# Kernel tuning notes

Measured on AMD Instinct MI355X. Metric: run time of the kernel, lower is better.

Reference implementation:

```python
import jax, jax.numpy as jnp
import numpy as np

# Constants from the torch module
S_DECAY = 0.95    # sentence_decay
P_DECAY = 0.99    # paragraph_decay
D_DECAY = 0.999   # document_decay
ALPHA = 0.1       # delta_update alpha for sentence/paragraph
DOC_ALPHA = 0.05  # delta_update alpha for document
BETA = 1.0
PARA_GROUP = 5    # sentences per paragraph
EPS = 1e-12       # F.normalize eps


def _normalize(x):
    # matches torch.nn.functional.normalize(x, dim=-1)
    return x / jnp.maximum(jnp.linalg.norm(x, axis=-1, keepdims=True), EPS)


def _delta_step(M, kn, v, alpha, beta):
    # M: [H, dk, dv]; kn: [dk] (already L2-normalized); v: [dv]
    # M_new = M @ (I - alpha * kn kn^T) + beta * kn v^T   (erase matrix is symmetric,
    # so the einsum 'hkv,hkj->hjv' form equals this rank-1 update -- no dk x dk matrix needed)
    kTM = jnp.einsum('k,hkv->hv', kn, M)                       # [H, dv]
    return M - alpha * kn[None, :, None] * kTM[:, None, :] \
             + beta * (kn[:, None] * v[None, :])[None, :, :]


def _scan_updates(M0, K, V, decay, alpha, beta):
    # Streaming delta-rule: per step, decay then erase/write.
    def step(M, kv):
        k, v = kv
        M = M * decay
        M = _delta_step(M, _normalize(k), v, alpha, beta)
        return M, None
    M, _ = jax.lax.scan(step, M0, (K, V))
    return M


def setup_inputs() -> dict:
    key = jax.random.key(0)
    ks = jax.random.split(key, 7)
    T, d_emb, d_k, d_v, H = 1000, 768, 256, 256, 8
    emb = jax.random.normal(ks[0], (T, d_emb), dtype=jnp.float32)
    q = jax.random.normal(ks[1], (d_k,), dtype=jnp.float32)
    W_k = jax.random.normal(ks[2], (d_emb, d_k), dtype=jnp.float32) * 0.02
    b_k = jax.random.normal(ks[3], (d_k,), dtype=jnp.float32) * 0.02
    W_v = jax.random.normal(ks[4], (d_emb, d_v), dtype=jnp.float32) * 0.02
    b_v = jax.random.normal(ks[5], (d_v,), dtype=jnp.float32) * 0.02
    M_sent0 = jnp.zeros((H, d_k, d_v), dtype=jnp.float32)
    M_para0 = jnp.zeros((H, d_k, d_v), dtype=jnp.float32)
    M_doc0 = jnp.zeros((H, d_k, d_v), dtype=jnp.float32)
    return {"emb": emb, "q": q, "W_k": W_k, "b_k": b_k, "W_v": W_v, "b_v": b_v,
            "M_sent0": M_sent0, "M_para0": M_para0, "M_doc0": M_doc0}


def reference(emb, q, W_k, b_k, W_v, b_v, M_sent0, M_para0, M_doc0):
    T, d_emb = emb.shape
    # Level 1: sentence memory -- one delta update per sentence embedding
    K = emb @ W_k + b_k            # [T, dk]
    V = emb @ W_v + b_v            # [T, dv]
    M_sent = _scan_updates(M_sent0, K, V, S_DECAY, ALPHA, BETA)
    # Level 2: paragraph memory -- mean of each group of 5 sentence embeddings
    para_emb = emb.reshape(T // PARA_GROUP, PARA_GROUP, d_emb).mean(axis=1)
    PK = para_emb @ W_k + b_k
    PV = para_emb @ W_v + b_v
    M_para = _scan_updates(M_para0, PK, PV, P_DECAY, ALPHA, BETA)
    # Level 3: document memory -- single update from paragraph-memory statistics
    doc_k = M_para.mean(axis=0).mean(axis=-1)   # [dk]
    doc_v = M_para.mean(axis=0).mean(axis=0)    # [dv]
    M_doc = M_doc0 * D_DECAY
    M_doc = _delta_step(M_doc, _normalize(doc_k), doc_v, DOC_ALPHA, BETA)
    # recall(q, level='all')
    qn = _normalize(q)
    def recall(M):
        return jnp.einsum('hkv,k->hv', M, qn).mean(axis=0)   # [dv]
    return 0.2 * recall(M_sent) + 0.3 * recall(M_para) + 0.5 * recall(M_doc)
```

## Files before the change

kernel.cpp:

```cpp
#include <hip/hip_runtime.h>
#include <hip/hip_bf16.h>

#define ALPHA   0.1f
#define S_DECAY 0.95f
#define P_DECAY 0.99f
#define D_EMB   768
#define DK      256

template<int ctrl, int row_mask>
__device__ __forceinline__ float dpp_add(float x) {
    int y = __builtin_amdgcn_update_dpp(0, __float_as_int(x), ctrl, row_mask, 0xF, true);
    return x + __int_as_float(y);
}

template<int N>
__device__ __forceinline__ void wave_allred_arr(float (&x)[N]) {
#pragma unroll
    for (int n = 0; n < N; ++n) x[n] = dpp_add<0xB1,  0xF>(x[n]);
#pragma unroll
    for (int n = 0; n < N; ++n) x[n] = dpp_add<0x4E,  0xF>(x[n]);
#pragma unroll
    for (int n = 0; n < N; ++n) x[n] = dpp_add<0x141, 0xF>(x[n]);
#pragma unroll
    for (int n = 0; n < N; ++n) x[n] = dpp_add<0x140, 0xF>(x[n]);
#pragma unroll
    for (int n = 0; n < N; ++n) x[n] = dpp_add<0x142, 0xA>(x[n]);
#pragma unroll
    for (int n = 0; n < N; ++n) x[n] = dpp_add<0x143, 0xC>(x[n]);
#pragma unroll
    for (int n = 0; n < N; ++n)
        x[n] = __int_as_float(__builtin_amdgcn_readlane(__float_as_int(x[n]), 63));
}

__device__ __forceinline__ float dot4v(const float4& a, const float4& b) {
    float t0 = a.x * b.x; t0 = fmaf(a.y, b.y, t0);
    float t1 = a.z * b.z; t1 = fmaf(a.w, b.w, t1);
    return t0 + t1;
}

__device__ __forceinline__ float rl(float x, int lane) {
    return __int_as_float(__builtin_amdgcn_readlane(__float_as_int(x), lane));
}

__global__ __launch_bounds__(256) void prep_kernel(
    const float* __restrict__ emb,
    const float* __restrict__ Wk, const float* __restrict__ bk,
    const float* __restrict__ Wv, const float* __restrict__ bv,
    float* __restrict__ K, float* __restrict__ V, float* __restrict__ USrev,
    float* __restrict__ out, int T)
{
    const int tid = threadIdx.x;
    const int bid = blockIdx.x;
    const int NBLK = (T / 4) * 2;
    if (bid >= NBLK) {
        const int PADS = ((T + 63) / 64) * 64;
        for (int i = tid; i < (PADS - T) * DK; i += 256) USrev[(size_t)T * DK + i] = 0.f;
        out[tid] = 0.f;
        return;
    }
    const int mat = bid & 1;
    const int r0  = (bid >> 1) * 4;

    __shared__ float se[4][D_EMB];
    __shared__ float s_red[4][4];

    const float4* emb4 = reinterpret_cast<const float4*>(emb);
#pragma unroll
    for (int r = 0; r < 4; ++r) {
        if (tid < D_EMB / 4)
            reinterpret_cast<float4*>(se[r])[tid] = emb4[(size_t)(r0 + r) * (D_EMB / 4) + tid];
    }
    __syncthreads();

    const float* Wp = mat ? Wv : Wk;
    const float* bp = mat ? bv : bk;
    const int j = tid;

    float a0 = 0.f, a1 = 0.f, a2 = 0.f, a3 = 0.f;
    float c0 = Wp[j],        c1 = Wp[j + DK],     c2 = Wp[j + 2*DK], c3 = Wp[j + 3*DK];
    float p0 = Wp[j + 4*DK], p1 = Wp[j + 5*DK],   p2 = Wp[j + 6*DK], p3 = Wp[j + 7*DK];

    for (int d = 0; d < D_EMB; d += 4) {
        int dn = d + 8; if (dn >= D_EMB) dn = 0;
        const float* wn = Wp + (size_t)dn * DK + j;
        float n0 = wn[0], n1 = wn[DK], n2 = wn[2*DK], n3 = wn[3*DK];

        float4 e0 = *reinterpret_cast<const float4*>(&se[0][d]);
        float4 e1 = *reinterpret_cast<const float4*>(&se[1][d]);
        float4 e2 = *reinterpret_cast<const float4*>(&se[2][d]);
        float4 e3 = *reinterpret_cast<const float4*>(&se[3][d]);

        a0 = fmaf(e0.x, c0, a0); a0 = fmaf(e0.y, c1, a0);
        a0 = fmaf(e0.z, c2, a0); a0 = fmaf(e0.w, c3, a0);
        a1 = fmaf(e1.x, c0, a1); a1 = fmaf(e1.y, c1, a1);
        a1 = fmaf(e1.z, c2, a1); a1 = fmaf(e1.w, c3, a1);
        a2 = fmaf(e2.x, c0, a2); a2 = fmaf(e2.y, c1, a2);
        a2 = fmaf(e2.z, c2, a2); a2 = fmaf(e2.w, c3, a2);
        a3 = fmaf(e3.x, c0, a3); a3 = fmaf(e3.y, c1, a3);
        a3 = fmaf(e3.z, c2, a3); a3 = fmaf(e3.w, c3, a3);

        c0 = p0; c1 = p1; c2 = p2; c3 = p3;
        p0 = n0; p1 = n1; p2 = n2; p3 = n3;
    }

    float bj = bp[j];
    float o0 = a0 + bj, o1 = a1 + bj, o2 = a2 + bj, o3 = a3 + bj;
    float* dst = mat ? V : K;
    dst[(size_t)(r0 + 0) * DK + j] = o0;
    dst[(size_t)(r0 + 1) * DK + j] = o1;
    dst[(size_t)(r0 + 2) * DK + j] = o2;
    dst[(size_t)(r0 + 3) * DK + j] = o3;

    if (mat == 0) {
        const int wave = tid >> 6, l = tid & 63;
        float red[4] = { o0*o0, o1*o1, o2*o2, o3*o3 };
        wave_allred_arr(red);
        if (l == 0) {
            s_red[wave][0] = red[0]; s_red[wave][1] = red[1];
            s_red[wave][2] = red[2]; s_red[wave][3] = red[3];
        }
        __syncthreads();
        float t0 = s_red[0][0] + s_red[1][0] + s_red[2][0] + s_red[3][0];
        float t1 = s_red[0][1] + s_red[1][1] + s_red[2][1] + s_red[3][1];
        float t2 = s_red[0][2] + s_red[1][2] + s_red[2][2] + s_red[3][2];
        float t3 = s_red[0][3] + s_red[1][3] + s_red[2][3] + s_red[3][3];
        USrev[(size_t)(T - 1 - (r0 + 0)) * DK + j] = o0 * (1.0f / fmaxf(sqrtf(t0), 1e-12f));
        USrev[(size_t)(T - 1 - (r0 + 1)) * DK + j] = o1 * (1.0f / fmaxf(sqrtf(t1), 1e-12f));
        USrev[(size_t)(T - 1 - (r0 + 2)) * DK + j] = o2 * (1.0f / fmaxf(sqrtf(t2), 1e-12f));
        USrev[(size_t)(T - 1 - (r0 + 3)) * DK + j] = o3 * (1.0f / fmaxf(sqrtf(t3), 1e-12f));
    }
}

__global__ __launch_bounds__(256) void graminv_kernel(
    const float* __restrict__ K, const float* __restrict__ V,
    const float* __restrict__ USrev,
    float* __restrict__ UPrev, float* __restrict__ UPfwd,
    float* __restrict__ PV, float* __restrict__ SVv,
    float* __restrict__ AinvT, float* __restrict__ biasF,
    int P, int NCS, int NCP)
{
    __shared__ float sU[64 * 257];
    __shared__ float sA[64 * 65];
    __shared__ float sX[64 * 65];
    __shared__ float s_sv[64];
    __shared__ float s_pd[64];
    const int tid = threadIdx.x, wv = tid >> 6, l = tid & 63;
    const int bid = blockIdx.x;
    int type, m;
    if (bid < NCS)            { type = 0; m = bid; }
    else if (bid < NCS + NCP) { type = 1; m = bid - NCS; }
    else                      { type = 2; m = bid - NCS - NCP; }

    if (tid < 64) s_pd[tid] = powf(P_DECAY, (float)tid);

    if (type == 0) {
        const float4* U4 = reinterpret_cast<const float4*>(USrev) + (size_t)m * 4096;
        for (int idx = tid; idx < 4096; idx += 256) {
            float4 t = U4[idx];
            int row = idx >> 6, c4 = (idx & 63) << 2;
            float* b = &sU[row * 257 + c4];
            b[0] = t.x; b[1] = t.y; b[2] = t.z; b[3] = t.w;
        }
    } else if (type == 1) {
        const float4* K4 = reinterpret_cast<const float4*>(K);
        for (int ii = 0; ii < 16; ++ii) {
            int i = wv * 16 + ii;
            int p = P - 1 - (64 * m + i);
            float4 u = make_float4(0.f, 0.f, 0.f, 0.f);
            if (p >= 0) {
                float4 pk = make_float4(0.f, 0.f, 0.f, 0.f);
#pragma unroll
                for (int s = 0; s < 5; ++s) {
                    float4 k4 = K4[(size_t)(5 * p + s) * 64 + l];
                    pk.x += k4.x; pk.y += k4.y; pk.z += k4.z; pk.w += k4.w;
                }
                pk.x *= 0.2f; pk.y *= 0.2f; pk.z *= 0.2f; pk.w *= 0.2f;
                float red[1] = { dot4v(pk, pk) };
                wave_allred_arr(red);
                float inv = 1.0f / fmaxf(sqrtf(red[0]), 1e-12f);
                u = make_float4(pk.x * inv, pk.y * inv, pk.z * inv, pk.w * inv);
            }
            float* b = &sU[i * 257 + 4 * l];
            b[0] = u.x; b[1] = u.y; b[2] = u.z; b[3] = u.w;
            reinterpret_cast<float4*>(UPrev)[(size_t)(64 * m + i) * 64 + l] = u;
        }
    } else {
        const float4* K4 = reinterpret_cast<const float4*>(K);
        const float4* V4 = reinterpret_cast<const float4*>(V);
        for (int ii = 0; ii < 16; ++ii) {
            int i = wv * 16 + ii;
            int p = 64 * m + i;
            float4 u = make_float4(0.f, 0.f, 0.f, 0.f);
            float sv = 0.f;
            if (p < P) {
                float4 pk = make_float4(0.f, 0.f, 0.f, 0.f);
                float4 pv = make_float4(0.f, 0.f, 0.f, 0.f);
#pragma unroll
                for (int s = 0; s < 5; ++s) {
                    float4 k4 = K4[(size_t)(5 * p + s) * 64 + l];
                    float4 v4 = V4[(size_t)(5 * p + s) * 64 + l];
                    pk.x += k4.x; pk.y += k4.y; pk.z += k4.z; pk.w += k4.w;
                    pv.x += v4.x; pv.y += v4.y; pv.z += v4.z; pv.w += v4.w;
                }
                pk.x *= 0.2f; pk.y *= 0.2f; pk.z *= 0.2f; pk.w *= 0.2f;
                pv.x *= 0.2f; pv.y *= 0.2f; pv.z *= 0.2f; pv.w *= 0.2f;
                reinterpret_cast<float4*>(PV)[(size_t)p * 64 + l] = pv;
                float red[2] = { dot4v(pk, pk), pv.x + pv.y + pv.z + pv.w };
                wave_allred_arr(red);
                float inv = 1.0f / fmaxf(sqrtf(red[0]), 1e-12f);
                u = make_float4(pk.x * inv, pk.y * inv, pk.z * inv, pk.w * inv);
                sv = red[1];
            }
            float* b = &sU[i * 257 + 4 * l];
            b[0] = u.x; b[1] = u.y; b[2] = u.z; b[3] = u.w;
            reinterpret_cast<float4*>(UPfwd)[(size_t)(64 * m + i) * 64 + l] = u;
            if (l == 0) { s_sv[i] = sv; SVv[64 * m + i] = sv; }
        }
    }
    __syncthreads();

    const int tr = tid & 15, tcg = tid >> 4;
    const int i0 = tr * 4, j0 = tcg * 4;
    float g00=0,g01=0,g02=0,g03=0, g10=0,g11=0,g12=0,g13=0;
    float g20=0,g21=0,g22=0,g23=0, g30=0,g31=0,g32=0,g33=0;
    for (int k = 0; k < 256; ++k) {
        float aa0 = sU[(i0    ) * 257 + k];
        float aa1 = sU[(i0 + 1) * 257 + k];
        float aa2 = sU[(i0 + 2) * 257 + k];
        float aa3 = sU[(i0 + 3) * 257 + k];
        float bb0 = sU[(j0    ) * 257 + k];
        float bb1 = sU[(j0 + 1) * 257 + k];
        float bb2 = sU[(j0 + 2) * 257 + k];
        float bb3 = sU[(j0 + 3) * 257 + k];
        g00 = fmaf(aa0, bb0, g00); g01 = fmaf(aa0, bb1, g01);
        g02 = fmaf(aa0, bb2, g02); g03 = fmaf(aa0, bb3, g03);
        g10 = fmaf(aa1, bb0, g10); g11 = fmaf(aa1, bb1, g11);
        g12 = fmaf(aa1, bb2, g12); g13 = fmaf(aa1, bb3, g13);
        g20 = fmaf(aa2, bb0, g20); g21 = fmaf(aa2, bb1, g21);
        g22 = fmaf(aa2, bb2, g22); g23 = fmaf(aa2, bb3, g23);
        g30 = fmaf(aa3, bb0, g30); g31 = fmaf(aa3, bb1, g31);
        g32 = fmaf(aa3, bb2, g32); g33 = fmaf(aa3, bb3, g33);
    }
    float gt[4][4] = { {g00,g01,g02,g03}, {g10,g11,g12,g13},
                       {g20,g21,g22,g23}, {g30,g31,g32,g33} };
#pragma unroll
    for (int r = 0; r < 4; ++r)
#pragma unroll
        for (int c = 0; c < 4; ++c) {
            int gi = i0 + r, gj = j0 + c;
            float val = 0.f;
            if (gj < gi) {
                val = ALPHA * gt[r][c];
                if (type == 2) val *= s_pd[gi - gj];
            }
            sA[gi * 65 + gj] = val;
        }
    __syncthreads();

    if (type == 2 && wv == 0) {
        float dotb = 0.f;
#pragma unroll
        for (int jj = 0; jj < 64; ++jj)
            dotb = fmaf(sA[l * 65 + jj], s_sv[jj], dotb);
        biasF[m * 64 + l] = dotb * (1.0f / ALPHA);
    }

    const int base = wv * 16;
    float x[16];
#pragma unroll
    for (int r = 0; r < 16; ++r) x[r] = (base + r == l) ? 1.f : 0.f;
    for (int s = 0; s < 4; ++s) {
        if (wv == s) {
#pragma unroll
            for (int i = 1; i < 16; ++i)
#pragma unroll
                for (int jj = 0; jj < 16; ++jj)
                    if (jj < i)
                        x[i] = fmaf(-sA[(base + i) * 65 + (base + jj)], x[jj], x[i]);
#pragma unroll
            for (int r = 0; r < 16; ++r) sX[(base + r) * 65 + l] = x[r];
        }
        __syncthreads();
        if (wv > s) {
#pragma unroll
            for (int i = 0; i < 16; ++i) {
                float xi = sX[(s * 16 + i) * 65 + l];
#pragma unroll
                for (int r = 0; r < 16; ++r)
                    x[r] = fmaf(-sA[(base + r) * 65 + (s * 16 + i)], xi, x[r]);
            }
        }
    }
    __syncthreads();
    float* dstA = AinvT + (size_t)bid * 4096;
    for (int idx = tid; idx < 4096; idx += 256) {
        int jcol = idx >> 6, irow = idx & 63;
        dstA[idx] = sX[irow * 65 + jcol];
    }
}

__global__ __launch_bounds__(256) void solve_kernel(
    const float* __restrict__ USrev, const float* __restrict__ UPrev,
    const float* __restrict__ UPfwd, const float* __restrict__ SVv,
    const float* __restrict__ AinvT, const float* __restrict__ biasF,
    const float* __restrict__ q,
    float* __restrict__ CS, float* __restrict__ CPB1, float* __restrict__ CPB2,
    float* __restrict__ gscal, int NCS, int NCP)
{
    __shared__ float s_b1[64], s_b2[64];
    __shared__ float4 s_part[4][64], s_part2[4][64];
    __shared__ float sAinv[4096];
    __shared__ float s_powd[65];
    const int tid = threadIdx.x, wave = tid >> 6, l = tid & 63;
    const int wbase = wave * 16;
    if (tid <= 64) s_powd[tid] = powf(P_DECAY, (float)tid);

    float4 q4 = reinterpret_cast<const float4*>(q)[l];
    float qs[1] = { dot4v(q4, q4) };
    wave_allred_arr(qs);
    float qinv = 1.0f / fmaxf(sqrtf(qs[0]), 1e-12f);
    float4 qn = make_float4(q4.x * qinv, q4.y * qinv, q4.z * qinv, q4.w * qinv);
    __syncthreads();

    const float4* G4 = reinterpret_cast<const float4*>(AinvT);
    float4* sAinv4 = reinterpret_cast<float4*>(sAinv);

    if (blockIdx.x == 0) {
        float4 w1 = qn;
        const float4* U4 = reinterpret_cast<const float4*>(USrev);
        float4 cur[16];
#pragma unroll
        for (int r = 0; r < 16; ++r) cur[r] = U4[(size_t)(wbase + r) * 64 + l];
        for (int m = 0; m < NCS; ++m) {
            float4 g0 = G4[(size_t)m * 1024 + 0*256 + tid];
            float4 g1 = G4[(size_t)m * 1024 + 1*256 + tid];
            float4 g2 = G4[(size_t)m * 1024 + 2*256 + tid];
            float4 g3 = G4[(size_t)m * 1024 + 3*256 + tid];
            float4 nxt[16];
            if (m + 1 < NCS) {
                const float4* Un = U4 + (size_t)(m + 1) * 64 * 64;
#pragma unroll
                for (int r = 0; r < 16; ++r) nxt[r] = Un[(size_t)(wbase + r) * 64 + l];
            }
#pragma unroll
            for (int g = 0; g < 4; ++g) {
                float d[4];
#pragma unroll
                for (int r = 0; r < 4; ++r) d[r] = dot4v(cur[g*4 + r], w1);
                wave_allred_arr(d);
                if (l == 0) {
                    int i0 = wbase + g*4;
                    s_b1[i0] = d[0]; s_b1[i0+1] = d[1]; s_b1[i0+2] = d[2]; s_b1[i0+3] = d[3];
                }
            }
            sAinv4[0*256 + tid] = g0;  sAinv4[1*256 + tid] = g1;
            sAinv4[2*256 + tid] = g2;  sAinv4[3*256 + tid] = g3;
            __syncthreads();
            float bv = s_b1[l];
            float c = 0.f;
#pragma unroll
            for (int jj = 0; jj < 64; ++jj)
                c = fmaf(sAinv[jj*64 + l], rl(bv, jj), c);
            if (wave == 0) CS[m * 64 + l] = c;
            float4 acc = make_float4(0.f, 0.f, 0.f, 0.f);
#pragma unroll
            for (int r = 0; r < 16; ++r) {
                float ci = rl(c, wbase + r);
                acc.x = fmaf(ci, cur[r].x, acc.x); acc.y = fmaf(ci, cur[r].y, acc.y);
                acc.z = fmaf(ci, cur[r].z, acc.z); acc.w = fmaf(ci, cur[r].w, acc.w);
            }
            s_part[wave][l] = acc;
            __syncthreads();
            float4 p0 = s_part[0][l], p1 = s_part[1][l], p2 = s_part[2][l], p3 = s_part[3][l];
            w1.x = fmaf(-ALPHA, p0.x + p1.x + p2.x + p3.x, w1.x);
            w1.y = fmaf(-ALPHA, p0.y + p1.y + p2.y + p3.y, w1.y);
            w1.z = fmaf(-ALPHA, p0.z + p1.z + p2.z + p3.z, w1.z);
            w1.w = fmaf(-ALPHA, p0.w + p1.w + p2.w + p3.w, w1.w);
            if (m + 1 < NCS) {
#pragma unroll
                for (int r = 0; r < 16; ++r) cur[r] = nxt[r];
            }
        }
    } else {
        {
            float4 w1 = qn;
            float4 w2 = make_float4(1.f, 1.f, 1.f, 1.f);
            const float4* U4 = reinterpret_cast<const float4*>(UPrev);
            float4 cur[16];
#pragma unroll
            for (int r = 0; r < 16; ++r) cur[r] = U4[(size_t)(wbase + r) * 64 + l];
            for (int m = 0; m < NCP; ++m) {
                size_t gb = (size_t)(NCS + m) * 1024;
                float4 g0 = G4[gb + 0*256 + tid];
                float4 g1 = G4[gb + 1*256 + tid];
                float4 g2 = G4[gb + 2*256 + tid];
                float4 g3 = G4[gb + 3*256 + tid];
                float4 nxt[16];
                if (m + 1 < NCP) {
                    const float4* Un = U4 + (size_t)(m + 1) * 64 * 64;
#pragma unroll
                    for (int r = 0; r < 16; ++r) nxt[r] = Un[(size_t)(wbase + r) * 64 + l];
                }
#pragma unroll
                for (int g = 0; g < 4; ++g) {
                    float d[8];
#pragma unroll
                    for (int r = 0; r < 4; ++r) {
                        d[r]     = dot4v(cur[g*4 + r], w1);
                        d[4 + r] = dot4v(cur[g*4 + r], w2);
                    }
                    wave_allred_arr(d);
                    if (l == 0) {
                        int i0 = wbase + g*4;
#pragma unroll
                        for (int r = 0; r < 4; ++r) { s_b1[i0+r] = d[r]; s_b2[i0+r] = d[4+r]; }
                    }
                }
                sAinv4[0*256 + tid] = g0;  sAinv4[1*256 + tid] = g1;
                sAinv4[2*256 + tid] = g2;  sAinv4[3*256 + tid] = g3;
                __syncthreads();
                float bv1 = s_b1[l], bv2 = s_b2[l];
                float c1 = 0.f, c2 = 0.f;
#pragma unroll
                for (int jj = 0; jj < 64; ++jj) {
                    float a = sAinv[jj*64 + l];
                    c1 = fmaf(a, rl(bv1, jj), c1);
                    c2 = fmaf(a, rl(bv2, jj), c2);
                }
                if (wave == 0) { CPB1[m * 64 + l] = c1; CPB2[m * 64 + l] = c2; }
                float4 a1 = make_float4(0.f,0.f,0.f,0.f), a2 = make_float4(0.f,0.f,0.f,0.f);
#pragma unroll
                for (int r = 0; r < 16; ++r) {
                    float x1 = rl(c1, wbase + r), x2 = rl(c2, wbase + r);
                    a1.x = fmaf(x1, cur[r].x, a1.x); a1.y = fmaf(x1, cur[r].y, a1.y);
                    a1.z = fmaf(x1, cur[r].z, a1.z); a1.w = fmaf(x1, cur[r].w, a1.w);
                    a2.x = fmaf(x2, cur[r].x, a2.x); a2.y = fmaf(x2, cur[r].y, a2.y);
                    a2.z = fmaf(x2, cur[r].z, a2.z); a2.w = fmaf(x2, cur[r].w, a2.w);
                }
                s_part[wave][l] = a1; s_part2[wave][l] = a2;
                __syncthreads();
                float4 p0 = s_part[0][l], p1 = s_part[1][l], p2 = s_part[2][l], p3 = s_part[3][l];
                w1.x = fmaf(-ALPHA, p0.x+p1.x+p2.x+p3.x, w1.x);
                w1.y = fmaf(-ALPHA, p0.y+p1.y+p2.y+p3.y, w1.y);
                w1.z = fmaf(-ALPHA, p0.z+p1.z+p2.z+p3.z, w1.z);
                w1.w = fmaf(-ALPHA, p0.w+p1.w+p2.w+p3.w, w1.w);
                float4 r0 = s_part2[0][l], r1 = s_part2[1][l], r2 = s_part2[2][l], r3 = s_part2[3][l];
                w2.x = fmaf(-ALPHA, r0.x+r1.x+r2.x+r3.x, w2.x);
                w2.y = fmaf(-ALPHA, r0.y+r1.y+r2.y+r3.y, w2.y);
                w2.z = fmaf(-ALPHA, r0.z+r1.z+r2.z+r3.z, w2.z);
                w2.w = fmaf(-ALPHA, r0.w+r1.w+r2.w+r3.w, w2.w);
                if (m + 1 < NCP) {
#pragma unroll
                    for (int r = 0; r < 16; ++r) cur[r] = nxt[r];
                }
            }
        }
        __syncthreads();
        float4 y = make_float4(0.f, 0.f, 0.f, 0.f);
        {
            const float4* U4 = reinterpret_cast<const float4*>(UPfwd);
            float4 cur[16];
#pragma unroll
            for (int r = 0; r < 16; ++r) cur[r] = U4[(size_t)(wbase + r) * 64 + l];
            for (int m = 0; m < NCP; ++m) {
                size_t gb = (size_t)(NCS + NCP + m) * 1024;
                float4 g0 = G4[gb + 0*256 + tid];
                float4 g1 = G4[gb + 1*256 + tid];
                float4 g2 = G4[gb + 2*256 + tid];
                float4 g3 = G4[gb + 3*256 + tid];
                float biasv = biasF[m * 64 + l];
                float svl   = SVv[m * 64 + l];
                float4 nxt[16];
                if (m + 1 < NCP) {
                    const float4* Un = U4 + (size_t)(m + 1) * 64 * 64;
#pragma unroll
                    for (int r = 0; r < 16; ++r) nxt[r] = Un[(size_t)(wbase + r) * 64 + l];
                }
#pragma unroll
                for (int g = 0; g < 4; ++g) {
                    float d[4];
#pragma unroll
                    for (int r = 0; r < 4; ++r) d[r] = dot4v(cur[g*4 + r], y);
                    wave_allred_arr(d);
                    if (l == 0) {
                        int i0 = wbase + g*4;
                        s_b1[i0] = d[0]; s_b1[i0+1] = d[1]; s_b1[i0+2] = d[2]; s_b1[i0+3] = d[3];
                    }
                }
                sAinv4[0*256 + tid] = g0;  sAinv4[1*256 + tid] = g1;
                sAinv4[2*256 + tid] = g2;  sAinv4[3*256 + tid] = g3;
                __syncthreads();
                float bvec = fmaf(s_powd[l + 1], s_b1[l], biasv);
                float c = 0.f;
#pragma unroll
                for (int jj = 0; jj < 64; ++jj)
                    c = fmaf(sAinv[jj*64 + l], rl(bvec, jj), c);
                float h = s_powd[63 - l] * fmaf(-ALPHA, c, svl);
                float4 acc = make_float4(0.f, 0.f, 0.f, 0.f);
#pragma unroll
                for (int r = 0; r < 16; ++r) {
                    float hi = rl(h, wbase + r);
                    acc.x = fmaf(hi, cur[r].x, acc.x); acc.y = fmaf(hi, cur[r].y, acc.y);
                    acc.z = fmaf(hi, cur[r].z, acc.z); acc.w = fmaf(hi, cur[r].w, acc.w);
                }
                s_part[wave][l] = acc;
                __syncthreads();
                float4 p0 = s_part[0][l], p1 = s_part[1][l], p2 = s_part[2][l], p3 = s_part[3][l];
                float d64 = s_powd[64];
                y.x = fmaf(d64, y.x, p0.x + p1.x + p2.x + p3.x);
                y.y = fmaf(d64, y.y, p0.y + p1.y + p2.y + p3.y);
                y.z = fmaf(d64, y.z, p0.z + p1.z + p2.z + p3.z);
                y.w = fmaf(d64, y.w, p0.w + p1.w + p2.w + p3.w);
                if (m + 1 < NCP) {
#pragma unroll
                    for (int r = 0; r < 16; ++r) cur[r] = nxt[r];
                }
            }
        }
        float fin[2] = { dot4v(y, y), dot4v(qn, y) };
        wave_allred_arr(fin);
        if (tid == 0) gscal[0] = fin[1] / fmaxf(sqrtf(fin[0]), 2.56e-10f);
    }
}

__global__ __launch_bounds__(256) void accum_kernel(
    const float* __restrict__ V, const float* __restrict__ PV,
    const float* __restrict__ CS, const float* __restrict__ CPB1,
    const float* __restrict__ CPB2, const float* __restrict__ gscal,
    float* __restrict__ out, int T, int P, int NCS, int NCP)
{
    __shared__ float wc[64];
    const int b = blockIdx.x, k = threadIdx.x;
    const float* src; const float* C; int i0, realN; float decay;
    if (b < NCS)            { src = V;  C = CS;   i0 = b * 64;               realN = T; decay = S_DECAY; }
    else if (b < NCS + NCP) { src = PV; C = CPB1; i0 = (b - NCS) * 64;       realN = P; decay = P_DECAY; }
    else                    { src = PV; C = CPB2; i0 = (b - NCS - NCP) * 64; realN = P; decay = P_DECAY; }
    if (k < 64) wc[k] = powf(decay, (float)(i0 + k)) * C[i0 + k];
    __syncthreads();
    float acc = 0.f;
    for (int ii = 0; ii < 64; ++ii) {
        int i = i0 + ii;
        if (i < realN)
            acc = fmaf(wc[ii], src[(size_t)(realN - 1 - i) * DK + k], acc);
    }
    float wlev;
    if (b < NCS)            wlev = 0.2f;
    else if (b < NCS + NCP) wlev = 0.3f;
    else                    wlev = (0.5f / 256.0f) * gscal[0];
    atomicAdd(&out[k], wlev * acc);
}

extern "C" void kernel_launch(void* const* d_in, const int* in_sizes, int n_in,
                              void* d_out, int out_size, void* d_ws, size_t ws_size,
                              hipStream_t stream) {
    const float* emb = (const float*)d_in[0];
    const float* q   = (const float*)d_in[1];
    const float* Wk  = (const float*)d_in[2];
    const float* bk  = (const float*)d_in[3];
    const float* Wv  = (const float*)d_in[4];
    const float* bv  = (const float*)d_in[5];

    const int T = in_sizes[0] / D_EMB;
    const int P = T / 5;
    const int NCS  = (T + 63) / 64;
    const int NCP  = (P + 63) / 64;
    const int PADS = NCS * 64;
    const int PADP = NCP * 64;

    float* ws    = (float*)d_ws;
    float* K     = ws;
    float* V     = K     + (size_t)T * DK;
    float* PV    = V     + (size_t)T * DK;
    float* USrev = PV    + (size_t)PADP * DK;
    float* UPrev = USrev + (size_t)PADS * DK;
    float* UPfwd = UPrev + (size_t)PADP * DK;
    float* SVv   = UPfwd + (size_t)PADP * DK;
    float* AinvT = SVv   + PADP;
    float* biasF = AinvT + (size_t)(NCS + 2*NCP) * 4096;
    float* CS    = biasF + PADP;
    float* CPB1  = CS    + PADS;
    float* CPB2  = CPB1  + PADP;
    float* gscal = CPB2  + PADP;

    prep_kernel<<<(T / 4) * 2 + 1, 256, 0, stream>>>(emb, Wk, bk, Wv, bv,
                                                     K, V, USrev, (float*)d_out, T);
    graminv_kernel<<<NCS + 2 * NCP, 256, 0, stream>>>(K, V, USrev, UPrev, UPfwd,
                                                      PV, SVv, AinvT, biasF, P, NCS, NCP);
    solve_kernel<<<2, 256, 0, stream>>>(USrev, UPrev, UPfwd, SVv, AinvT, biasF, q,
                                        CS, CPB1, CPB2, gscal, NCS, NCP);
    accum_kernel<<<NCS + 2 * NCP, 256, 0, stream>>>(V, PV, CS, CPB1, CPB2, gscal,
                                                    (float*)d_out, T, P, NCS, NCP);
}
```

Before: 192.2 us.

## Precompute per-chunk W = Ainv·U in parallel kernel to shorten serial solve loop

```diff
diff --git a/kernel.cpp b/kernel.cpp
--- a/kernel.cpp
+++ b/kernel.cpp
@@ -36,10 +36,6 @@
     float t0 = a.x * b.x; t0 = fmaf(a.y, b.y, t0);
     float t1 = a.z * b.z; t1 = fmaf(a.w, b.w, t1);
     return t0 + t1;
-}
-
-__device__ __forceinline__ float rl(float x, int lane) {
-    return __int_as_float(__builtin_amdgcn_readlane(__float_as_int(x), lane));
 }
 
 __global__ __launch_bounds__(256) void prep_kernel(
@@ -136,7 +132,8 @@
     const float* __restrict__ USrev,
     float* __restrict__ UPrev, float* __restrict__ UPfwd,
     float* __restrict__ PV, float* __restrict__ SVv,
-    float* __restrict__ AinvT, float* __restrict__ biasF,
+    float* __restrict__ AinvT, float* __restrict__ Wall,
+    float* __restrict__ F1, float* __restrict__ biasF,
     int P, int NCS, int NCP)
 {
     __shared__ float sU[64 * 257];
@@ -144,6 +141,8 @@
     __shared__ float sX[64 * 65];
     __shared__ float s_sv[64];
     __shared__ float s_pd[64];
+    __shared__ float4 s_f1[4];
+    __shared__ float4 s_f1w[4][64];
     const int tid = threadIdx.x, wv = tid >> 6, l = tid & 63;
     const int bid = blockIdx.x;
     int type, m;
@@ -152,6 +151,8 @@
     else                      { type = 2; m = bid - NCS - NCP; }
 
     if (tid < 64) s_pd[tid] = powf(P_DECAY, (float)tid);
+
+    float4 f1p = make_float4(0.f, 0.f, 0.f, 0.f);
 
     if (type == 0) {
         const float4* U4 = reinterpret_cast<const float4*>(USrev) + (size_t)m * 4096;
@@ -215,46 +216,59 @@
             b[0] = u.x; b[1] = u.y; b[2] = u.z; b[3] = u.w;
             reinterpret_cast<float4*>(UPfwd)[(size_t)(64 * m + i) * 64 + l] = u;
             if (l == 0) { s_sv[i] = sv; SVv[64 * m + i] = sv; }
-        }
-    }
-    __syncthreads();
+            float f = powf(P_DECAY, (float)(63 - i)) * sv;
+            f1p.x = fmaf(f, u.x, f1p.x); f1p.y = fmaf(f, u.y, f1p.y);
+            f1p.z = fmaf(f, u.z, f1p.z); f1p.w = fmaf(f, u.w, f1p.w);
+        }
+        s_f1w[wv][l] = f1p;
+    }
+    __syncthreads();
+
+    if (type == 2 && wv == 0) {
+        float4 a = s_f1w[0][l], b = s_f1w[1][l], c = s_f1w[2][l], d = s_f1w[3][l];
+        float4 tot = make_float4(a.x+b.x+c.x+d.x, a.y+b.y+c.y+d.y,
+                                 a.z+b.z+c.z+d.z, a.w+b.w+c.w+d.w);
+        reinterpret_cast<float4*>(F1)[(size_t)m * 64 + l] = tot;
+    }
 
     const int tr = tid & 15, tcg = tid >> 4;
     const int i0 = tr * 4, j0 = tcg * 4;
-    float g00=0,g01=0,g02=0,g03=0, g10=0,g11=0,g12=0,g13=0;
-    float g20=0,g21=0,g22=0,g23=0, g30=0,g31=0,g32=0,g33=0;
-    for (int k = 0; k < 256; ++k) {
-        float aa0 = sU[(i0    ) * 257 + k];
-        float aa1 = sU[(i0 + 1) * 257 + k];
-        float aa2 = sU[(i0 + 2) * 257 + k];
-        float aa3 = sU[(i0 + 3) * 257 + k];
-        float bb0 = sU[(j0    ) * 257 + k];
-        float bb1 = sU[(j0 + 1) * 257 + k];
-        float bb2 = sU[(j0 + 2) * 257 + k];
-        float bb3 = sU[(j0 + 3) * 257 + k];
-        g00 = fmaf(aa0, bb0, g00); g01 = fmaf(aa0, bb1, g01);
-        g02 = fmaf(aa0, bb2, g02); g03 = fmaf(aa0, bb3, g03);
-        g10 = fmaf(aa1, bb0, g10); g11 = fmaf(aa1, bb1, g11);
-        g12 = fmaf(aa1, bb2, g12); g13 = fmaf(aa1, bb3, g13);
-        g20 = fmaf(aa2, bb0, g20); g21 = fmaf(aa2, bb1, g21);
-        g22 = fmaf(aa2, bb2, g22); g23 = fmaf(aa2, bb3, g23);
-        g30 = fmaf(aa3, bb0, g30); g31 = fmaf(aa3, bb1, g31);
-        g32 = fmaf(aa3, bb2, g32); g33 = fmaf(aa3, bb3, g33);
-    }
-    float gt[4][4] = { {g00,g01,g02,g03}, {g10,g11,g12,g13},
-                       {g20,g21,g22,g23}, {g30,g31,g32,g33} };
-#pragma unroll
-    for (int r = 0; r < 4; ++r)
-#pragma unroll
-        for (int c = 0; c < 4; ++c) {
-            int gi = i0 + r, gj = j0 + c;
-            float val = 0.f;
-            if (gj < gi) {
-                val = ALPHA * gt[r][c];
-                if (type == 2) val *= s_pd[gi - gj];
-            }
-            sA[gi * 65 + gj] = val;
-        }
+    {
+        float g00=0,g01=0,g02=0,g03=0, g10=0,g11=0,g12=0,g13=0;
+        float g20=0,g21=0,g22=0,g23=0, g30=0,g31=0,g32=0,g33=0;
+        for (int k = 0; k < 256; ++k) {
+            float aa0 = sU[(i0    ) * 257 + k];
+            float aa1 = sU[(i0 + 1) * 257 + k];
+            float aa2 = sU[(i0 + 2) * 257 + k];
+            float aa3 = sU[(i0 + 3) * 257 + k];
+            float bb0 = sU[(j0    ) * 257 + k];
+            float bb1 = sU[(j0 + 1) * 257 + k];
+            float bb2 = sU[(j0 + 2) * 257 + k];
+            float bb3 = sU[(j0 + 3) * 257 + k];
+            g00 = fmaf(aa0, bb0, g00); g01 = fmaf(aa0, bb1, g01);
+            g02 = fmaf(aa0, bb2, g02); g03 = fmaf(aa0, bb3, g03);
+            g10 = fmaf(aa1, bb0, g10); g11 = fmaf(aa1, bb1, g11);
+            g12 = fmaf(aa1, bb2, g12); g13 = fmaf(aa1, bb3, g13);
+            g20 = fmaf(aa2, bb0, g20); g21 = fmaf(aa2, bb1, g21);
+            g22 = fmaf(aa2, bb2, g22); g23 = fmaf(aa2, bb3, g23);
+            g30 = fmaf(aa3, bb0, g30); g31 = fmaf(aa3, bb1, g31);
+            g32 = fmaf(aa3, bb2, g32); g33 = fmaf(aa3, bb3, g33);
+        }
+        float gt[4][4] = { {g00,g01,g02,g03}, {g10,g11,g12,g13},
+                           {g20,g21,g22,g23}, {g30,g31,g32,g33} };
+#pragma unroll
+        for (int r = 0; r < 4; ++r)
+#pragma unroll
+            for (int c = 0; c < 4; ++c) {
+                int gi = i0 + r, gj = j0 + c;
+                float val = 0.f;
+                if (gj < gi) {
+                    val = ALPHA * gt[r][c];
+                    if (type == 2) val *= s_pd[gi - gj];
+                }
+                sA[gi * 65 + gj] = val;
+            }
+    }
     __syncthreads();
 
     if (type == 2 && wv == 0) {
@@ -265,54 +279,94 @@
         biasF[m * 64 + l] = dotb * (1.0f / ALPHA);
     }
 
-    const int base = wv * 16;
-    float x[16];
-#pragma unroll
-    for (int r = 0; r < 16; ++r) x[r] = (base + r == l) ? 1.f : 0.f;
-    for (int s = 0; s < 4; ++s) {
-        if (wv == s) {
-#pragma unroll
-            for (int i = 1; i < 16; ++i)
-#pragma unroll
-                for (int jj = 0; jj < 16; ++jj)
-                    if (jj < i)
-                        x[i] = fmaf(-sA[(base + i) * 65 + (base + jj)], x[jj], x[i]);
-#pragma unroll
-            for (int r = 0; r < 16; ++r) sX[(base + r) * 65 + l] = x[r];
-        }
-        __syncthreads();
-        if (wv > s) {
-#pragma unroll
-            for (int i = 0; i < 16; ++i) {
-                float xi = sX[(s * 16 + i) * 65 + l];
-#pragma unroll
-                for (int r = 0; r < 16; ++r)
-                    x[r] = fmaf(-sA[(base + r) * 65 + (s * 16 + i)], xi, x[r]);
-            }
-        }
-    }
-    __syncthreads();
-    float* dstA = AinvT + (size_t)bid * 4096;
-    for (int idx = tid; idx < 4096; idx += 256) {
-        int jcol = idx >> 6, irow = idx & 63;
-        dstA[idx] = sX[irow * 65 + jcol];
-    }
-}
-
-__global__ __launch_bounds__(256) void solve_kernel(
+    {
+        const int base = wv * 16;
+        float x[16];
+#pragma unroll
+        for (int r = 0; r < 16; ++r) x[r] = (base + r == l) ? 1.f : 0.f;
+        for (int s = 0; s < 4; ++s) {
+            if (wv == s) {
+#pragma unroll
+                for (int i = 1; i < 16; ++i)
+#pragma unroll
+                    for (int jj = 0; jj < 16; ++jj)
+                        if (jj < i)
+                            x[i] = fmaf(-sA[(base + i) * 65 + (base + jj)], x[jj], x[i]);
+#pragma unroll
+                for (int r = 0; r < 16; ++r) sX[(base + r) * 65 + l] = x[r];
+            }
+            __syncthreads();
+            if (wv > s) {
+#pragma unroll
+                for (int i = 0; i < 16; ++i) {
+                    float xi = sX[(s * 16 + i) * 65 + l];
+#pragma unroll
+                    for (int r = 0; r < 16; ++r)
+                        x[r] = fmaf(-sA[(base + r) * 65 + (s * 16 + i)], xi, x[r]);
+                }
+            }
+        }
+    }
+    __syncthreads();
+
+    if (type != 2) {
+        float* dstA = AinvT + (size_t)bid * 4096;
+        for (int idx = tid; idx < 4096; idx += 256) {
+            int jcol = idx >> 6, irow = idx & 63;
+            dstA[idx] = sX[irow * 65 + jcol];
+        }
+    }
+
+    {
+        const int c0 = tcg * 16;
+        float wacc[4][16];
+#pragma unroll
+        for (int r = 0; r < 4; ++r)
+#pragma unroll
+            for (int c = 0; c < 16; ++c) wacc[r][c] = 0.f;
+        for (int i = 0; i < 64; ++i) {
+            float x0 = sX[i * 65 + i0    ];
+            float x1 = sX[i * 65 + i0 + 1];
+            float x2 = sX[i * 65 + i0 + 2];
+            float x3 = sX[i * 65 + i0 + 3];
+            if (type == 2) {
+                float f = s_pd[63 - i];
+                x0 *= f; x1 *= f; x2 *= f; x3 *= f;
+            }
+#pragma unroll
+            for (int c = 0; c < 16; ++c) {
+                float u = sU[i * 257 + c0 + c];
+                wacc[0][c] = fmaf(x0, u, wacc[0][c]);
+                wacc[1][c] = fmaf(x1, u, wacc[1][c]);
+                wacc[2][c] = fmaf(x2, u, wacc[2][c]);
+                wacc[3][c] = fmaf(x3, u, wacc[3][c]);
+            }
+        }
+        float* dstW = Wall + (size_t)bid * 16384;
+#pragma unroll
+        for (int r = 0; r < 4; ++r) {
+#pragma unroll
+            for (int c4 = 0; c4 < 4; ++c4) {
+                float4 t = make_float4(wacc[r][c4*4], wacc[r][c4*4+1],
+                                       wacc[r][c4*4+2], wacc[r][c4*4+3]);
+                reinterpret_cast<float4*>(dstW)[((i0 + r) * 256 + c0 + c4*4) >> 2] = t;
+            }
+        }
+    }
+}
+
+__global__ __launch_bounds__(512) void solve_kernel(
     const float* __restrict__ USrev, const float* __restrict__ UPrev,
-    const float* __restrict__ UPfwd, const float* __restrict__ SVv,
-    const float* __restrict__ AinvT, const float* __restrict__ biasF,
+    const float* __restrict__ UPfwd, const float* __restrict__ Wall,
+    const float* __restrict__ F1, const float* __restrict__ biasF,
     const float* __restrict__ q,
-    float* __restrict__ CS, float* __restrict__ CPB1, float* __restrict__ CPB2,
+    float* __restrict__ BS, float* __restrict__ BPB1, float* __restrict__ BPB2,
     float* __restrict__ gscal, int NCS, int NCP)
 {
-    __shared__ float s_b1[64], s_b2[64];
-    __shared__ float4 s_part[4][64], s_part2[4][64];
-    __shared__ float sAinv[4096];
+    __shared__ float4 s_part[2][8][64], s_part2[2][8][64];
     __shared__ float s_powd[65];
     const int tid = threadIdx.x, wave = tid >> 6, l = tid & 63;
-    const int wbase = wave * 16;
+    const int wb = wave * 8;
     if (tid <= 64) s_powd[tid] = powf(P_DECAY, (float)tid);
 
     float4 q4 = reinterpret_cast<const float4*>(q)[l];
@@ -322,63 +376,54 @@
     float4 qn = make_float4(q4.x * qinv, q4.y * qinv, q4.z * qinv, q4.w * qinv);
     __syncthreads();
 
-    const float4* G4 = reinterpret_cast<const float4*>(AinvT);
-    float4* sAinv4 = reinterpret_cast<float4*>(sAinv);
+    const float4* W4 = reinterpret_cast<const float4*>(Wall);
 
     if (blockIdx.x == 0) {
         float4 w1 = qn;
         const float4* U4 = reinterpret_cast<const float4*>(USrev);
-        float4 cur[16];
-#pragma unroll
-        for (int r = 0; r < 16; ++r) cur[r] = U4[(size_t)(wbase + r) * 64 + l];
+        float4 curU[8];
+#pragma unroll
+        for (int r = 0; r < 8; ++r) curU[r] = U4[(size_t)(wb + r) * 64 + l];
         for (int m = 0; m < NCS; ++m) {
-            float4 g0 = G4[(size_t)m * 1024 + 0*256 + tid];
-            float4 g1 = G4[(size_t)m * 1024 + 1*256 + tid];
-            float4 g2 = G4[(size_t)m * 1024 + 2*256 + tid];
-            float4 g3 = G4[(size_t)m * 1024 + 3*256 + tid];
-            float4 nxt[16];
+            float4 curW[8];
+#pragma unroll
+            for (int r = 0; r < 8; ++r)
+                curW[r] = W4[(size_t)m * 4096 + (size_t)(wb + r) * 64 + l];
+            float4 nxtU[8];
             if (m + 1 < NCS) {
-                const float4* Un = U4 + (size_t)(m + 1) * 64 * 64;
-#pragma unroll
-                for (int r = 0; r < 16; ++r) nxt[r] = Un[(size_t)(wbase + r) * 64 + l];
-            }
-#pragma unroll
-            for (int g = 0; g < 4; ++g) {
-                float d[4];
-#pragma unroll
-                for (int r = 0; r < 4; ++r) d[r] = dot4v(cur[g*4 + r], w1);
-                wave_allred_arr(d);
-                if (l == 0) {
-                    int i0 = wbase + g*4;
-                    s_b1[i0] = d[0]; s_b1[i0+1] = d[1]; s_b1[i0+2] = d[2]; s_b1[i0+3] = d[3];
-                }
-            }
-            sAinv4[0*256 + tid] = g0;  sAinv4[1*256 + tid] = g1;
-            sAinv4[2*256 + tid] = g2;  sAinv4[3*256 + tid] = g3;
+#pragma unroll
+                for (int r = 0; r < 8; ++r)
+                    nxtU[r] = U4[(size_t)(m + 1) * 4096 + (size_t)(wb + r) * 64 + l];
+            }
+            float d[8];
+#pragma unroll
+            for (int r = 0; r < 8; ++r) d[r] = dot4v(curU[r], w1);
+            wave_allred_arr(d);
+            if (l == 0) {
+#pragma unroll
+                for (int r = 0; r < 8; ++r) BS[m * 64 + wb + r] = d[r];
+            }
+            float4 part = make_float4(0.f, 0.f, 0.f, 0.f);
+#pragma unroll
+            for (int r = 0; r < 8; ++r) {
+                part.x = fmaf(d[r], curW[r].x, part.x);
+                part.y = fmaf(d[r], curW[r].y, part.y);
+                part.z = fmaf(d[r], curW[r].z, part.z);
+                part.w = fmaf(d[r], curW[r].w, part.w);
+            }
+            s_part[m & 1][wave][l] = part;
             __syncthreads();
-            float bv = s_b1[l];
-            float c = 0.f;
-#pragma unroll
-            for (int jj = 0; jj < 64; ++jj)
-                c = fmaf(sAinv[jj*64 + l], rl(bv, jj), c);
-            if (wave == 0) CS[m * 64 + l] = c;
-            float4 acc = make_float4(0.f, 0.f, 0.f, 0.f);
-#pragma unroll
-            for (int r = 0; r < 16; ++r) {
-                float ci = rl(c, wbase + r);
-                acc.x = fmaf(ci, cur[r].x, acc.x); acc.y = fmaf(ci, cur[r].y, acc.y);
-                acc.z = fmaf(ci, cur[r].z, acc.z); acc.w = fmaf(ci, cur[r].w, acc.w);
-            }
-            s_part[wave][l] = acc;
-            __syncthreads();
-            float4 p0 = s_part[0][l], p1 = s_part[1][l], p2 = s_part[2][l], p3 = s_part[3][l];
-            w1.x = fmaf(-ALPHA, p0.x + p1.x + p2.x + p3.x, w1.x);
-            w1.y = fmaf(-ALPHA, p0.y + p1.y + p2.y + p3.y, w1.y);
-            w1.z = fmaf(-ALPHA, p0.z + p1.z + p2.z + p3.z, w1.z);
-            w1.w = fmaf(-ALPHA, p0.w + p1.w + p2.w + p3.w, w1.w);
+            float4 s = make_float4(0.f, 0.f, 0.f, 0.f);
+#pragma unroll
+            for (int w = 0; w < 8; ++w) {
+                float4 p = s_part[m & 1][w][l];
+                s.x += p.x; s.y += p.y; s.z += p.z; s.w += p.w;
+            }
+            w1.x = fmaf(-ALPHA, s.x, w1.x); w1.y = fmaf(-ALPHA, s.y, w1.y);
+            w1.z = fmaf(-ALPHA, s.z, w1.z); w1.w = fmaf(-ALPHA, s.w, w1.w);
             if (m + 1 < NCS) {
 #pragma unroll
-                for (int r = 0; r < 16; ++r) cur[r] = nxt[r];
+                for (int r = 0; r < 8; ++r) curU[r] = nxtU[r];
             }
         }
     } else {
@@ -386,72 +431,58 @@
             float4 w1 = qn;
             float4 w2 = make_float4(1.f, 1.f, 1.f, 1.f);
             const float4* U4 = reinterpret_cast<const float4*>(UPrev);
-            float4 cur[16];
-#pragma unroll
-            for (int r = 0; r < 16; ++r) cur[r] = U4[(size_t)(wbase + r) * 64 + l];
+            float4 curU[8];
+#pragma unroll
+            for (int r = 0; r < 8; ++r) curU[r] = U4[(size_t)(wb + r) * 64 + l];
             for (int m = 0; m < NCP; ++m) {
-                size_t gb = (size_t)(NCS + m) * 1024;
-                float4 g0 = G4[gb + 0*256 + tid];
-                float4 g1 = G4[gb + 1*256 + tid];
-                float4 g2 = G4[gb + 2*256 + tid];
-                float4 g3 = G4[gb + 3*256 + tid];
-                float4 nxt[16];
+                float4 curW[8];
+#pragma unroll
+                for (int r = 0; r < 8; ++r)
+                    curW[r] = W4[(size_t)(NCS + m) * 4096 + (size_t)(wb + r) * 64 + l];
+                float4 nxtU[8];
                 if (m + 1 < NCP) {
-                    const float4* Un = U4 + (size_t)(m + 1) * 64 * 64;
-#pragma unroll
-                    for (int r = 0; r < 16; ++r) nxt[r] = Un[(size_t)(wbase + r) * 64 + l];
-                }
-#pragma unroll
-                for (int g = 0; g < 4; ++g) {
-                    float d[8];
-#pragma unroll
-                    for (int r = 0; r < 4; ++r) {
-                        d[r]     = dot4v(cur[g*4 + r], w1);
-                        d[4 + r] = dot4v(cur[g*4 + r], w2);
+#pragma unroll
+                    for (int r = 0; r < 8; ++r)
+                        nxtU[r] = U4[(size_t)(m + 1) * 4096 + (size_t)(wb + r) * 64 + l];
+                }
+                float d[16];
+#pragma unroll
+                for (int r = 0; r < 8; ++r) {
+                    d[r]     = dot4v(curU[r], w1);
+                    d[8 + r] = dot4v(curU[r], w2);
+                }
+                wave_allred_arr(d);
+                if (l == 0) {
+#pragma unroll
+                    for (int r = 0; r < 8; ++r) {
+                        BPB1[m * 64 + wb + r] = d[r];
+                        BPB2[m * 64 + wb + r] = d[8 + r];
                     }
-                    wave_allred_arr(d);
-                    if (l == 0) {
-                        int i0 = wbase + g*4;
-#pragma unroll
-                        for (int r = 0; r < 4; ++r) { s_b1[i0+r] = d[r]; s_b2[i0+r] = d[4+r]; }
-                    }
-                }
-                sAinv4[0*256 + tid] = g0;  sAinv4[1*256 + tid] = g1;
-                sAinv4[2*256 + tid] = g2;  sAinv4[3*256 + tid] = g3;
+                }
+                float4 p1 = make_float4(0.f,0.f,0.f,0.f), p2 = make_float4(0.f,0.f,0.f,0.f);
+#pragma unroll
+                for (int r = 0; r < 8; ++r) {
+                    p1.x = fmaf(d[r], curW[r].x, p1.x);   p1.y = fmaf(d[r], curW[r].y, p1.y);
+                    p1.z = fmaf(d[r], curW[r].z, p1.z);   p1.w = fmaf(d[r], curW[r].w, p1.w);
+                    p2.x = fmaf(d[8+r], curW[r].x, p2.x); p2.y = fmaf(d[8+r], curW[r].y, p2.y);
+                    p2.z = fmaf(d[8+r], curW[r].z, p2.z); p2.w = fmaf(d[8+r], curW[r].w, p2.w);
+                }
+                s_part[m & 1][wave][l] = p1; s_part2[m & 1][wave][l] = p2;
                 __syncthreads();
-                float bv1 = s_b1[l], bv2 = s_b2[l];
-                float c1 = 0.f, c2 = 0.f;
-#pragma unroll
-                for (int jj = 0; jj < 64; ++jj) {
-                    float a = sAinv[jj*64 + l];
-                    c1 = fmaf(a, rl(bv1, jj), c1);
-                    c2 = fmaf(a, rl(bv2, jj), c2);
-                }
-                if (wave == 0) { CPB1[m * 64 + l] = c1; CPB2[m * 64 + l] = c2; }
-                float4 a1 = make_float4(0.f,0.f,0.f,0.f), a2 = make_float4(0.f,0.f,0.f,0.f);
-#pragma unroll
-                for (int r = 0; r < 16; ++r) {
-                    float x1 = rl(c1, wbase + r), x2 = rl(c2, wbase + r);
-                    a1.x = fmaf(x1, cur[r].x, a1.x); a1.y = fmaf(x1, cur[r].y, a1.y);
-                    a1.z = fmaf(x1, cur[r].z, a1.z); a1.w = fmaf(x1, cur[r].w, a1.w);
-                    a2.x = fmaf(x2, cur[r].x, a2.x); a2.y = fmaf(x2, cur[r].y, a2.y);
-                    a2.z = fmaf(x2, cur[r].z, a2.z); a2.w = fmaf(x2, cur[r].w, a2.w);
-                }
-                s_part[wave][l] = a1; s_part2[wave][l] = a2;
-                __syncthreads();
-                float4 p0 = s_part[0][l], p1 = s_part[1][l], p2 = s_part[2][l], p3 = s_part[3][l];
-                w1.x = fmaf(-ALPHA, p0.x+p1.x+p2.x+p3.x, w1.x);
-                w1.y = fmaf(-ALPHA, p0.y+p1.y+p2.y+p3.y, w1.y);
-                w1.z = fmaf(-ALPHA, p0.z+p1.z+p2.z+p3.z, w1.z);
-                w1.w = fmaf(-ALPHA, p0.w+p1.w+p2.w+p3.w, w1.w);
-                float4 r0 = s_part2[0][l], r1 = s_part2[1][l], r2 = s_part2[2][l], r3 = s_part2[3][l];
-                w2.x = fmaf(-ALPHA, r0.x+r1.x+r2.x+r3.x, w2.x);
-                w2.y = fmaf(-ALPHA, r0.y+r1.y+r2.y+r3.y, w2.y);
-                w2.z = fmaf(-ALPHA, r0.z+r1.z+r2.z+r3.z, w2.z);
-                w2.w = fmaf(-ALPHA, r0.w+r1.w+r2.w+r3.w, w2.w);
+                float4 s1 = make_float4(0.f,0.f,0.f,0.f), s2 = make_float4(0.f,0.f,0.f,0.f);
+#pragma unroll
+                for (int w = 0; w < 8; ++w) {
+                    float4 a = s_part[m & 1][w][l];  float4 b = s_part2[m & 1][w][l];
+                    s1.x += a.x; s1.y += a.y; s1.z += a.z; s1.w += a.w;
+                    s2.x += b.x; s2.y += b.y; s2.z += b.z; s2.w += b.w;
+                }
+                w1.x = fmaf(-ALPHA, s1.x, w1.x); w1.y = fmaf(-ALPHA, s1.y, w1.y);
+                w1.z = fmaf(-ALPHA, s1.z, w1.z); w1.w = fmaf(-ALPHA, s1.w, w1.w);
+                w2.x = fmaf(-ALPHA, s2.x, w2.x); w2.y = fmaf(-ALPHA, s2.y, w2.y);
+                w2.z = fmaf(-ALPHA, s2.z, w2.z); w2.w = fmaf(-ALPHA, s2.w, w2.w);
                 if (m + 1 < NCP) {
 #pragma unroll
-                    for (int r = 0; r < 16; ++r) cur[r] = nxt[r];
+                    for (int r = 0; r < 8; ++r) curU[r] = nxtU[r];
                 }
             }
         }
@@ -459,61 +490,55 @@
         float4 y = make_float4(0.f, 0.f, 0.f, 0.f);
         {
             const float4* U4 = reinterpret_cast<const float4*>(UPfwd);
-            float4 cur[16];
-#pragma unroll
-            for (int r = 0; r < 16; ++r) cur[r] = U4[(size_t)(wbase + r) * 64 + l];
+            float4 curU[8];
+#pragma unroll
+            for (int r = 0; r < 8; ++r) curU[r] = U4[(size_t)(wb + r) * 64 + l];
             for (int m = 0; m < NCP; ++m) {
-                size_t gb = (size_t)(NCS + NCP + m) * 1024;
-                float4 g0 = G4[gb + 0*256 + tid];
-                float4 g1 = G4[gb + 1*256 + tid];
-                float4 g2 = G4[gb + 2*256 + tid];
-                float4 g3 = G4[gb + 3*256 + tid];
-                float biasv = biasF[m * 64 + l];
-                float svl   = SVv[m * 64 + l];
-                float4 nxt[16];
+                float4 curW[8];
+#pragma unroll
+                for (int r = 0; r < 8; ++r)
+                    curW[r] = W4[(size_t)(NCS + NCP + m) * 4096 + (size_t)(wb + r) * 64 + l];
+                float biasr[8];
+#pragma unroll
+                for (int r = 0; r < 8; ++r) biasr[r] = biasF[m * 64 + wb + r];
+                float4 f1 = reinterpret_cast<const float4*>(F1)[(size_t)m * 64 + l];
+                float4 nxtU[8];
                 if (m + 1 < NCP) {
-                    const float4* Un = U4 + (size_t)(m + 1) * 64 * 64;
-#pragma unroll
-                    for (int r = 0; r < 16; ++r) nxt[r] = Un[(size_t)(wbase + r) * 64 + l];
-                }
-#pragma unroll
-                for (int g = 0; g < 4; ++g) {
-                    float d[4];
-#pragma unroll
-                    for (int r = 0; r < 4; ++r) d[r] = dot4v(cur[g*4 + r], y);
-                    wave_allred_arr(d);
-                    if (l == 0) {
-                        int i0 = wbase + g*4;
-                        s_b1[i0] = d[0]; s_b1[i0+1] = d[1]; s_b1[i0+2] = d[2]; s_b1[i0+3] = d[3];
-                    }
-                }
-                sAinv4[0*256 + tid] = g0;  sAinv4[1*256 + tid] = g1;
-                sAinv4[2*256 + tid] = g2;  sAinv4[3*256 + tid] = g3;
+#pragma unroll
+                    for (int r = 0; r < 8; ++r)
+                        nxtU[r] = U4[(size_t)(m + 1) * 4096 + (size_t)(wb + r) * 64 + l];
+                }
+                float d[8];
+#pragma unroll
+                for (int r = 0; r < 8; ++r) d[r] = dot4v(curU[r], y);
+                wave_allred_arr(d);
+#pragma unroll
+                for (int r = 0; r < 8; ++r)
+                    d[r] = fmaf(s_powd[wb + r + 1], d[r], biasr[r]);
+                float4 part = make_float4(0.f, 0.f, 0.f, 0.f);
+#pragma unroll
+                for (int r = 0; r < 8; ++r) {
+                    part.x = fmaf(d[r], curW[r].x, part.x);
+                    part.y = fmaf(d[r], curW[r].y, part.y);
+                    part.z = fmaf(d[r], curW[r].z, part.z);
+                    part.w = fmaf(d[r], curW[r].w, part.w);
+                }
+                s_part[m & 1][wave][l] = part;
                 __syncthreads();
-                float bvec = fmaf(s_powd[l + 1], s_b1[l], biasv);
-                float c = 0.f;
-#pragma unroll
-                for (int jj = 0; jj < 64; ++jj)
-                    c = fmaf(sAinv[jj*64 + l], rl(bvec, jj), c);
-                float h = s_powd[63 - l] * fmaf(-ALPHA, c, svl);
-                float4 acc = make_float4(0.f, 0.f, 0.f, 0.f);
-#pragma unroll
-                for (int r = 0; r < 16; ++r) {
-                    float hi = rl(h, wbase + r);
-                    acc.x = fmaf(hi, cur[r].x, acc.x); acc.y = fmaf(hi, cur[r].y, acc.y);
-                    acc.z = fmaf(hi, cur[r].z, acc.z); acc.w = fmaf(hi, cur[r].w, acc.w);
-                }
-                s_part[wave][l] = acc;
-                __syncthreads();
-                float4 p0 = s_part[0][l], p1 = s_part[1][l], p2 = s_part[2][l], p3 = s_part[3][l];
+                float4 s = make_float4(0.f, 0.f, 0.f, 0.f);
+#pragma unroll
+                for (int w = 0; w < 8; ++w) {
+                    float4 p = s_part[m & 1][w][l];
+                    s.x += p.x; s.y += p.y; s.z += p.z; s.w += p.w;
+                }
                 float d64 = s_powd[64];
-                y.x = fmaf(d64, y.x, p0.x + p1.x + p2.x + p3.x);
-                y.y = fmaf(d64, y.y, p0.y + p1.y + p2.y + p3.y);
-                y.z = fmaf(d64, y.z, p0.z + p1.z + p2.z + p3.z);
-                y.w = fmaf(d64, y.w, p0.w + p1.w + p2.w + p3.w);
+                y.x = fmaf(d64, y.x, fmaf(-ALPHA, s.x, f1.x));
+                y.y = fmaf(d64, y.y, fmaf(-ALPHA, s.y, f1.y));
+                y.z = fmaf(d64, y.z, fmaf(-ALPHA, s.z, f1.z));
+                y.w = fmaf(d64, y.w, fmaf(-ALPHA, s.w, f1.w));
                 if (m + 1 < NCP) {
 #pragma unroll
-                    for (int r = 0; r < 16; ++r) cur[r] = nxt[r];
+                    for (int r = 0; r < 8; ++r) curU[r] = nxtU[r];
                 }
             }
         }
@@ -525,18 +550,38 @@
 
 __global__ __launch_bounds__(256) void accum_kernel(
     const float* __restrict__ V, const float* __restrict__ PV,
-    const float* __restrict__ CS, const float* __restrict__ CPB1,
-    const float* __restrict__ CPB2, const float* __restrict__ gscal,
+    const float* __restrict__ AinvT,
+    const float* __restrict__ BS, const float* __restrict__ BPB1,
+    const float* __restrict__ BPB2, const float* __restrict__ gscal,
     float* __restrict__ out, int T, int P, int NCS, int NCP)
 {
-    __shared__ float wc[64];
-    const int b = blockIdx.x, k = threadIdx.x;
-    const float* src; const float* C; int i0, realN; float decay;
-    if (b < NCS)            { src = V;  C = CS;   i0 = b * 64;               realN = T; decay = S_DECAY; }
-    else if (b < NCS + NCP) { src = PV; C = CPB1; i0 = (b - NCS) * 64;       realN = P; decay = P_DECAY; }
-    else                    { src = PV; C = CPB2; i0 = (b - NCS - NCP) * 64; realN = P; decay = P_DECAY; }
-    if (k < 64) wc[k] = powf(decay, (float)(i0 + k)) * C[i0 + k];
-    __syncthreads();
+    __shared__ float s_b[64], s_cp[4][64], wc[64];
+    const int b = blockIdx.x, t = threadIdx.x;
+    const float* src; const float* B; int i0, realN, chunk; float decay;
+    if (b < NCS)            { src = V;  B = BS;   i0 = b * 64;               realN = T; decay = S_DECAY; chunk = b; }
+    else if (b < NCS + NCP) { src = PV; B = BPB1; i0 = (b - NCS) * 64;       realN = P; decay = P_DECAY; chunk = b; }
+    else                    { src = PV; B = BPB2; i0 = (b - NCS - NCP) * 64; realN = P; decay = P_DECAY; chunk = b - NCP; }
+    if (t < 64) s_b[t] = B[(i0 & ~63) + t - i0 + i0];
+    if (t < 64) s_b[t] = B[((b < NCS) ? b : (b < NCS + NCP ? b - NCS : b - NCS - NCP)) * 64 + t];
+    __syncthreads();
+    {
+        const int part = t >> 6, k = t & 63;
+        const float* Xc = AinvT + (size_t)chunk * 4096;
+        float cp = 0.f;
+#pragma unroll
+        for (int jj = 0; jj < 16; ++jj) {
+            int j = part * 16 + jj;
+            cp = fmaf(Xc[j * 64 + k], s_b[j], cp);
+        }
+        s_cp[part][k] = cp;
+    }
+    __syncthreads();
+    if (t < 64) {
+        float c = s_cp[0][t] + s_cp[1][t] + s_cp[2][t] + s_cp[3][t];
+        wc[t] = powf(decay, (float)(i0 + t)) * c;
+    }
+    __syncthreads();
+    const int k = t;
     float acc = 0.f;
     for (int ii = 0; ii < 64; ++ii) {
         int i = i0 + ii;
@@ -566,6 +611,7 @@
     const int NCP  = (P + 63) / 64;
     const int PADS = NCS * 64;
     const int PADP = NCP * 64;
+    const int NCH  = NCS + 2 * NCP;
 
     float* ws    = (float*)d_ws;
     float* K     = ws;
@@ -576,18 +622,20 @@
     float* UPfwd = UPrev + (size_t)PADP * DK;
     float* SVv   = UPfwd + (size_t)PADP * DK;
     float* AinvT = SVv   + PADP;
-    float* biasF = AinvT + (size_t)(NCS + 2*NCP) * 4096;
-    float* CS    = biasF + PADP;
-    float* CPB1  = CS    + PADS;
-    float* CPB2  = CPB1  + PADP;
-    float* gscal = CPB2  + PADP;
+    float* Wall  = AinvT + (size_t)NCH * 4096;
+    float* F1    = Wall  + (size_t)NCH * 16384;
+    float* biasF = F1    + (size_t)NCP * 256;
+    float* BS    = biasF + PADP;
+    float* BPB1  = BS    + PADS;
+    float* BPB2  = BPB1  + PADP;
+    float* gscal = BPB2  + PADP;
 
     prep_kernel<<<(T / 4) * 2 + 1, 256, 0, stream>>>(emb, Wk, bk, Wv, bv,
                                                      K, V, USrev, (float*)d_out, T);
-    graminv_kernel<<<NCS + 2 * NCP, 256, 0, stream>>>(K, V, USrev, UPrev, UPfwd,
-                                                      PV, SVv, AinvT, biasF, P, NCS, NCP);
-    solve_kernel<<<2, 256, 0, stream>>>(USrev, UPrev, UPfwd, SVv, AinvT, biasF, q,
-                                        CS, CPB1, CPB2, gscal, NCS, NCP);
-    accum_kernel<<<NCS + 2 * NCP, 256, 0, stream>>>(V, PV, CS, CPB1, CPB2, gscal,
-                                                    (float*)d_out, T, P, NCS, NCP);
-}
+    graminv_kernel<<<NCH, 256, 0, stream>>>(K, V, USrev, UPrev, UPfwd,
+                                            PV, SVv, AinvT, Wall, F1, biasF, P, NCS, NCP);
+    solve_kernel<<<2, 512, 0, stream>>>(USrev, UPrev, UPfwd, Wall, F1, biasF, q,
+                                        BS, BPB1, BPB2, gscal, NCS, NCP);
+    accum_kernel<<<NCH, 256, 0, stream>>>(V, PV, AinvT, BS, BPB1, BPB2, gscal,
+                                          (float*)d_out, T, P, NCS, NCP);
+}
```

Result: slower. 198.4 us (+3.2%).
